# Kernel tuning notes

Hardware: AMD Instinct MI355X
Metric: run time of the kernel (lower is better)

The kernel has to match this reference:

```python
import jax, jax.numpy as jnp
import numpy as np

H = 8      # num_heads
DH = 80    # head_dim = embed_dim // num_heads


def setup_inputs() -> dict:
    key = jax.random.key(0)
    ks = jax.random.split(key, 7)
    B, T, S = 8, 4096, 77
    hidden, embed, ctx = 640, 640, 768
    sc_h = 1.0 / np.sqrt(hidden)
    sc_c = 1.0 / np.sqrt(ctx)
    sc_e = 1.0 / np.sqrt(embed)
    return {
        "tokens": jax.random.normal(ks[0], (B, T, hidden), jnp.float32),
        "context": jax.random.normal(ks[1], (B, S, ctx), jnp.float32),
        "Wq": jax.random.normal(ks[2], (hidden, embed), jnp.float32) * sc_h,
        "Wk": jax.random.normal(ks[3], (ctx, embed), jnp.float32) * sc_c,
        "Wv": jax.random.normal(ks[4], (ctx, embed), jnp.float32) * sc_c,
        "Wo": jax.random.normal(ks[5], (embed, hidden), jnp.float32) * sc_e,
        "bo": jnp.zeros((hidden,), jnp.float32),
    }


def reference(tokens, context, Wq, Wk, Wv, Wo, bo):
    B, T, _ = tokens.shape
    S = context.shape[1]
    Q = (tokens @ Wq).reshape(B, T, H, DH)    # B T H D
    K = (context @ Wk).reshape(B, S, H, DH)   # B S H D
    V = (context @ Wv).reshape(B, S, H, DH)
    scores = jnp.einsum('bthd,bshd->bhts', Q, K) / jnp.sqrt(jnp.float32(DH))
    attn = jax.nn.softmax(scores, axis=-1)    # B H T S
    ctx_vecs = jnp.einsum('bhts,bshd->bthd', attn, V).reshape(B, T, H * DH)
    return ctx_vecs @ Wo + bo
```

## Files before the change

kernel.cpp:

```cpp
#include <hip/hip_runtime.h>
#include <hip/hip_bf16.h>
#include <hip/hip_fp16.h>

typedef __attribute__((ext_vector_type(4))) float f32x4;
typedef __attribute__((ext_vector_type(8))) _Float16 f16x8;
typedef __attribute__((ext_vector_type(8))) unsigned short u16x8;

__device__ __forceinline__ unsigned short f2h(float f) {
    _Float16 h = (_Float16)f;
    return __builtin_bit_cast(unsigned short, h);
}

#define GLOAD_LDS16(gp, lp) __builtin_amdgcn_global_load_lds( \
    (const __attribute__((address_space(1))) void*)(gp), \
    (__attribute__((address_space(3))) void*)(lp), 16, 0, 0)
#define PRIO1() __builtin_amdgcn_s_setprio(1)
#define PRIO0() __builtin_amdgcn_s_setprio(0)

__global__ void cvt_kernel(const float* __restrict__ in, ushort* __restrict__ out, int n4) {
    int stride = gridDim.x * blockDim.x;
    for (int i = blockIdx.x * blockDim.x + threadIdx.x; i < n4; i += stride) {
        float4 v = ((const float4*)in)[i];
        ushort4 o;
        o.x = f2h(v.x); o.y = f2h(v.y); o.z = f2h(v.z); o.w = f2h(v.w);
        ((ushort4*)out)[i] = o;
    }
}

__global__ void transpose_cvt2(const float* __restrict__ Wk, const float* __restrict__ Wv,
                               ushort* __restrict__ WkvT) {
    __shared__ float tile[32][33];
    const int z = blockIdx.z;
    const float* src = z ? Wv : Wk;
    ushort* dst = WkvT + (size_t)z * 640 * 768;
    const int R = 768, C = 640;
    int tx = threadIdx.x, ty = threadIdx.y;
    int c = blockIdx.x * 32 + tx;
    int r0 = blockIdx.y * 32;
#pragma unroll
    for (int i = ty; i < 32; i += 8) {
        int r = r0 + i;
        tile[i][tx] = (r < R && c < C) ? src[(size_t)r * C + c] : 0.f;
    }
    __syncthreads();
    int rr = r0 + tx;
    int c0 = blockIdx.x * 32;
#pragma unroll
    for (int i = ty; i < 32; i += 8) {
        int cc = c0 + i;
        if (cc < C && rr < R) dst[(size_t)cc * R + rr] = f2h(tile[tx][i]);
    }
}

__global__ void pack_wfrag(const float* __restrict__ W, ushort* __restrict__ WF) {
    int g = blockIdx.x * 256 + threadIdx.x;
    if (g >= 51200) return;
    int lane = g & 63;
    int fi = (g >> 6) % 10;
    int kt = ((g >> 6) / 10) % 10;
    int h  = (g >> 6) / 100;
    int ni = fi >> 1, kk = fi & 1;
    int n  = h * 80 + ni * 16 + (lane & 15);
    int k0 = kt * 64 + kk * 32 + (lane >> 4) * 8;
    u16x8 o;
#pragma unroll
    for (int e = 0; e < 8; ++e) o[e] = f2h(W[(size_t)(k0 + e) * 640 + n]);
    *(u16x8*)&WF[(size_t)g * 8] = o;
}

__global__ void pack_kvfrag(const ushort* __restrict__ KVb,
                            ushort* __restrict__ KF, ushort* __restrict__ VF) {
    int g = blockIdx.x * 256 + threadIdx.x;
    if (g >= 61440) return;
    int lane = g & 63;
    int fi = (g >> 6) % 15;
    int bh = (g >> 6) / 15;
    int b = bh >> 3, h = bh & 7;
    int ni = fi / 3, kk = fi % 3;
    int l15 = lane & 15, lhi = lane >> 4;
    int sr = ni * 16 + l15; if (sr > 76) sr = 76;
    int d0 = kk * 32 + lhi * 8;
    u16x8 ko, vo;
#pragma unroll
    for (int e = 0; e < 8; ++e)
        ko[e] = KVb[((size_t)b * 77 + sr) * 1280 + h * 80 + d0 + e];
    int dv = ni * 16 + l15;
    int s0 = kk * 32 + lhi * 8;
#pragma unroll
    for (int e = 0; e < 8; ++e) {
        int s = s0 + e;
        vo[e] = (s < 77) ? KVb[((size_t)b * 77 + s) * 1280 + 640 + h * 80 + dv] : (ushort)0;
    }
    *(u16x8*)&KF[(size_t)g * 8] = ko;
    *(u16x8*)&VF[(size_t)g * 8] = vo;
}

template<int OUT_F16, int HAS_BIAS>
__global__ __launch_bounds__(256) void gemm_bt(
    const ushort* __restrict__ A, const ushort* __restrict__ Bt,
    void* __restrict__ C, const float* __restrict__ bias,
    int M, int N, int K)
{
    __shared__ ushort As[128 * 64];
    __shared__ ushort Bs[128 * 64];
    const int tid = threadIdx.x;
    const int lane = tid & 63;
    const int w = tid >> 6;
    const int wr = (w >> 1) * 64, wc = (w & 1) * 64;
    const int m0 = blockIdx.x * 128, n0 = blockIdx.y * 128;
    const int l15 = lane & 15, lhi = lane >> 4;

    f32x4 acc[4][4] = {};

    for (int k0 = 0; k0 < K; k0 += 64) {
        __syncthreads();
#pragma unroll
        for (int i = 0; i < 4; ++i) {
            int c = i * 256 + tid;
            int m = m0 + (c >> 3);
            if (m > M - 1) m = M - 1;
            GLOAD_LDS16(A + (size_t)m * K + k0 + (c & 7) * 8, &As[c * 8]);
        }
#pragma unroll
        for (int i = 0; i < 4; ++i) {
            int c = i * 256 + tid;
            GLOAD_LDS16(Bt + (size_t)(n0 + (c >> 3)) * K + k0 + (c & 7) * 8, &Bs[c * 8]);
        }
        __syncthreads();
#pragma unroll
        for (int kk = 0; kk < 2; ++kk) {
            f16x8 af[4], bfr[4];
#pragma unroll
            for (int mi = 0; mi < 4; ++mi)
                af[mi] = *(const f16x8*)&As[(wr + mi * 16 + l15) * 64 + kk * 32 + lhi * 8];
#pragma unroll
            for (int ni = 0; ni < 4; ++ni)
                bfr[ni] = *(const f16x8*)&Bs[(wc + ni * 16 + l15) * 64 + kk * 32 + lhi * 8];
#pragma unroll
            for (int mi = 0; mi < 4; ++mi)
#pragma unroll
                for (int ni = 0; ni < 4; ++ni)
                    acc[mi][ni] = __builtin_amdgcn_mfma_f32_16x16x32_f16(
                        af[mi], bfr[ni], acc[mi][ni], 0, 0, 0);
        }
    }

#pragma unroll
    for (int mi = 0; mi < 4; ++mi)
#pragma unroll
        for (int ni = 0; ni < 4; ++ni)
#pragma unroll
            for (int r = 0; r < 4; ++r) {
                int row = m0 + wr + mi * 16 + lhi * 4 + r;
                int col = n0 + wc + ni * 16 + l15;
                if (row < M) {
                    float v = acc[mi][ni][r];
                    if (HAS_BIAS) v += bias[col];
                    if (OUT_F16) ((ushort*)C)[(size_t)row * N + col] = f2h(v);
                    else         ((float*)C)[(size_t)row * N + col] = v;
                }
            }
}

__global__ __launch_bounds__(512, 2) void fused_attn(
    const float* __restrict__ tokens, const ushort* __restrict__ WqF,
    const ushort* __restrict__ KF, const ushort* __restrict__ VF,
    const ushort* __restrict__ WoF, const float* __restrict__ bo,
    float* __restrict__ out)
{
    __shared__ __align__(16) ushort lds[40960];
    const int tid = threadIdx.x;
    const int lane = tid & 63;
    const int w = tid >> 6;
    const int l15 = lane & 15, lhi = lane >> 4;
    const int tt = blockIdx.x, b = blockIdx.y;
    const size_t rowbase = (size_t)b * 4096 + (size_t)tt * 64;

    const ushort* WqFb = WqF + (size_t)w * 10 * 5120;
    const ushort* WoFb = WoF + (size_t)w * 10 * 5120;
    const ushort* KFb  = KF + (size_t)(b * 8 + w) * 15 * 512;
    const ushort* VFb  = VF + (size_t)(b * 8 + w) * 15 * 512;

    const int srow = tid >> 3;
    const int sc8  = tid & 7;
    {
        const float* tbase = tokens + (rowbase + srow) * 640 + sc8 * 8;
        float4 sA[4], sB[4];
#pragma unroll
        for (int kt = 0; kt < 4; ++kt) {
            sA[kt] = ((const float4*)(tbase + kt * 64))[0];
            sB[kt] = ((const float4*)(tbase + kt * 64))[1];
        }
#pragma unroll
        for (int kt = 0; kt < 10; ++kt) {
            const int sl = kt & 3;
            u16x8 o;
            o[0]=f2h(sA[sl].x); o[1]=f2h(sA[sl].y); o[2]=f2h(sA[sl].z); o[3]=f2h(sA[sl].w);
            o[4]=f2h(sB[sl].x); o[5]=f2h(sB[sl].y); o[6]=f2h(sB[sl].z); o[7]=f2h(sB[sl].w);
            *(u16x8*)&lds[srow * 640 + (kt * 8 + (sc8 ^ (srow & 7))) * 8] = o;
            if (kt + 4 < 10) {
                sA[sl] = ((const float4*)(tbase + (kt + 4) * 64))[0];
                sB[sl] = ((const float4*)(tbase + (kt + 4) * 64))[1];
            }
        }
    }
    f16x8 BbE[10], BbO[10];
#pragma unroll
    for (int f = 0; f < 10; ++f)
        BbE[f] = *(const f16x8*)(WqFb + f * 512 + lane * 8);
    __syncthreads();

    f32x4 qacc[4][5] = {};
#define QSTEP(BCUR, BNXT, KT) do { \
    const int kt_ = (KT); \
    if (kt_ < 9) { \
        _Pragma("unroll") for (int f = 0; f < 10; ++f) \
            (BNXT)[f] = *(const f16x8*)(WqFb + (size_t)(kt_+1)*5120 + f*512 + lane*8); \
    } \
    _Pragma("unroll") for (int kk = 0; kk < 2; ++kk) { \
        f16x8 af[4]; \
        _Pragma("unroll") for (int mi = 0; mi < 4; ++mi) { \
            int row_ = mi*16 + l15; \
            af[mi] = *(const f16x8*)&lds[row_*640 + (kt_*8 + ((kk*4 + lhi) ^ (row_ & 7)))*8]; \
        } \
        PRIO1(); \
        _Pragma("unroll") for (int mi = 0; mi < 4; ++mi) \
        _Pragma("unroll") for (int ni = 0; ni < 5; ++ni) \
            qacc[mi][ni] = __builtin_amdgcn_mfma_f32_16x16x32_f16(af[mi], (BCUR)[ni*2+kk], qacc[mi][ni], 0, 0, 0); \
        PRIO0(); \
    } \
} while (0)
    for (int kp = 0; kp < 5; ++kp) {
        QSTEP(BbE, BbO, 2*kp);
        QSTEP(BbO, BbE, 2*kp + 1);
    }
#undef QSTEP
    __syncthreads();

    const int qoff = w * 5120;
#pragma unroll
    for (int mi = 0; mi < 4; ++mi)
#pragma unroll
        for (int ni = 0; ni < 5; ++ni)
#pragma unroll
            for (int r = 0; r < 4; ++r)
                lds[qoff + (mi*16 + lhi*4 + r)*80 + ni*16 + l15] = f2h(qacc[mi][ni][r]);
    __builtin_amdgcn_sched_barrier(0);

    const f16x8 zf = {};
    f32x4 sa[4][5] = {};
    {
        f16x8 bk[15];
#pragma unroll
        for (int f = 0; f < 15; ++f)
            bk[f] = *(const f16x8*)(KFb + f * 512 + lane * 8);
#pragma unroll
        for (int kk = 0; kk < 3; ++kk) {
            f16x8 aq[4];
            const int kcol = (kk < 2) ? (kk*32 + lhi*8) : (64 + (lhi & 1)*8);
#pragma unroll
            for (int mi = 0; mi < 4; ++mi) {
                aq[mi] = *(const f16x8*)&lds[qoff + (mi*16 + l15)*80 + kcol];
                if (kk == 2 && lhi >= 2) aq[mi] = zf;
            }
            PRIO1();
#pragma unroll
            for (int mi = 0; mi < 4; ++mi)
#pragma unroll
                for (int ni = 0; ni < 5; ++ni)
                    sa[mi][ni] = __builtin_amdgcn_mfma_f32_16x16x32_f16(aq[mi], bk[ni*3+kk], sa[mi][ni], 0, 0, 0);
            PRIO0();
        }
    }
    __builtin_amdgcn_sched_barrier(0);

    const float sc = 0.11180339887498949f;
#pragma unroll
    for (int mi = 0; mi < 4; ++mi)
#pragma unroll
        for (int r = 0; r < 4; ++r) {
            float v0 = sa[mi][0][r]*sc, v1 = sa[mi][1][r]*sc, v2 = sa[mi][2][r]*sc,
                  v3 = sa[mi][3][r]*sc, v4 = sa[mi][4][r]*sc;
            bool ok4 = l15 < 13;
            float mx = fmaxf(fmaxf(v0, v1), fmaxf(v2, v3));
            if (ok4) mx = fmaxf(mx, v4);
#pragma unroll
            for (int off = 1; off < 16; off <<= 1) mx = fmaxf(mx, __shfl_xor(mx, off, 16));
            float p0 = __expf(v0-mx), p1 = __expf(v1-mx), p2 = __expf(v2-mx), p3 = __expf(v3-mx);
            float p4 = ok4 ? __expf(v4-mx) : 0.f;
            float sm = p0+p1+p2+p3+p4;
#pragma unroll
            for (int off = 1; off < 16; off <<= 1) sm += __shfl_xor(sm, off, 16);
            float inv = 1.f / sm;
            int row = mi*16 + lhi*4 + r;
            lds[qoff + row*80 + 0*16 + l15] = f2h(p0*inv);
            lds[qoff + row*80 + 1*16 + l15] = f2h(p1*inv);
            lds[qoff + row*80 + 2*16 + l15] = f2h(p2*inv);
            lds[qoff + row*80 + 3*16 + l15] = f2h(p3*inv);
            lds[qoff + row*80 + 4*16 + l15] = f2h(p4*inv);
        }
    __builtin_amdgcn_sched_barrier(0);

    f32x4 oa[4][5] = {};
    {
        f16x8 bv[15];
#pragma unroll
        for (int f = 0; f < 15; ++f)
            bv[f] = *(const f16x8*)(VFb + f * 512 + lane * 8);
#pragma unroll
        for (int kk = 0; kk < 3; ++kk) {
            f16x8 ap[4];
            const int kcol = (kk < 2) ? (kk*32 + lhi*8) : (64 + (lhi & 1)*8);
#pragma unroll
            for (int mi = 0; mi < 4; ++mi) {
                ap[mi] = *(const f16x8*)&lds[qoff + (mi*16 + l15)*80 + kcol];
                if (kk == 2 && lhi >= 2) ap[mi] = zf;
            }
            PRIO1();
#pragma unroll
            for (int mi = 0; mi < 4; ++mi)
#pragma unroll
                for (int ni = 0; ni < 5; ++ni)
                    oa[mi][ni] = __builtin_amdgcn_mfma_f32_16x16x32_f16(ap[mi], bv[ni*3+kk], oa[mi][ni], 0, 0, 0);
            PRIO0();
        }
    }
    __syncthreads();

#pragma unroll
    for (int mi = 0; mi < 4; ++mi)
#pragma unroll
        for (int ni = 0; ni < 5; ++ni)
#pragma unroll
            for (int r = 0; r < 4; ++r) {
                int row = mi*16 + lhi*4 + r;
                int col = w*80 + ni*16 + l15;
                int slot = col >> 3;
                int phys = (((slot & ~7) | ((slot ^ row) & 7)) << 3) | (col & 7);
                lds[row*640 + phys] = f2h(oa[mi][ni][r]);
            }
    __syncthreads();

    f32x4 cacc[4][5] = {};
#pragma unroll
    for (int f = 0; f < 10; ++f)
        BbE[f] = *(const f16x8*)(WoFb + f * 512 + lane * 8);
#define OSTEP(BCUR, BNXT, KT) do { \
    const int kt_ = (KT); \
    if (kt_ < 9) { \
        _Pragma("unroll") for (int f = 0; f < 10; ++f) \
            (BNXT)[f] = *(const f16x8*)(WoFb + (size_t)(kt_+1)*5120 + f*512 + lane*8); \
    } \
    _Pragma("unroll") for (int kk = 0; kk < 2; ++kk) { \
        f16x8 af[4]; \
        _Pragma("unroll") for (int mi = 0; mi < 4; ++mi) { \
            int row_ = mi*16 + l15; \
            af[mi] = *(const f16x8*)&lds[row_*640 + (kt_*8 + ((kk*4 + lhi) ^ (row_ & 7)))*8]; \
        } \
        PRIO1(); \
        _Pragma("unroll") for (int mi = 0; mi < 4; ++mi) \
        _Pragma("unroll") for (int ni = 0; ni < 5; ++ni) \
            cacc[mi][ni] = __builtin_amdgcn_mfma_f32_16x16x32_f16(af[mi], (BCUR)[ni*2+kk], cacc[mi][ni], 0, 0, 0); \
        PRIO0(); \
    } \
} while (0)
    for (int kp = 0; kp < 5; ++kp) {
        OSTEP(BbE, BbO, 2*kp);
        OSTEP(BbO, BbE, 2*kp + 1);
    }
#undef OSTEP

#pragma unroll
    for (int ni = 0; ni < 5; ++ni) {
        int col = w*80 + ni*16 + l15;
        float bvl = bo[col];
#pragma unroll
        for (int mi = 0; mi < 4; ++mi)
#pragma unroll
            for (int r = 0; r < 4; ++r)
                out[(rowbase + mi*16 + lhi*4 + r) * 640 + col] = cacc[mi][ni][r] + bvl;
    }
}

extern "C" void kernel_launch(void* const* d_in, const int* in_sizes, int n_in,
                              void* d_out, int out_size, void* d_ws, size_t ws_size,
                              hipStream_t stream) {
    (void)in_sizes; (void)n_in; (void)out_size; (void)ws_size;
    const float* tokens  = (const float*)d_in[0];
    const float* context = (const float*)d_in[1];
    const float* Wq = (const float*)d_in[2];
    const float* Wk = (const float*)d_in[3];
    const float* Wv = (const float*)d_in[4];
    const float* Wo = (const float*)d_in[5];
    const float* bo = (const float*)d_in[6];
    float* out = (float*)d_out;

    ushort* ws   = (ushort*)d_ws;
    ushort* ctx16 = ws;
    ushort* WkvT = ctx16 + (size_t)616 * 768;
    ushort* KVb  = WkvT + (size_t)1280 * 768;
    ushort* WqF  = KVb  + (size_t)616 * 1280;
    ushort* WoF  = WqF  + (size_t)640 * 640;
    ushort* KF   = WoF  + (size_t)640 * 640;
    ushort* VF   = KF   + (size_t)61440 * 8;

    cvt_kernel<<<462, 256, 0, stream>>>(context, ctx16, 616 * 768 / 4);
    transpose_cvt2<<<dim3(20, 24, 2), dim3(32, 8), 0, stream>>>(Wk, Wv, WkvT);
    pack_wfrag<<<200, 256, 0, stream>>>(Wq, WqF);
    pack_wfrag<<<200, 256, 0, stream>>>(Wo, WoF);
    gemm_bt<1, 0><<<dim3(5, 10), 256, 0, stream>>>(ctx16, WkvT, KVb, nullptr, 616, 1280, 768);
    pack_kvfrag<<<240, 256, 0, stream>>>(KVb, KF, VF);
    fused_attn<<<dim3(64, 8), 512, 0, stream>>>(tokens, WqF, KF, VF, WoF, bo, out);
}
```

Measured before the change: 123.6 us.

## Halve fused attention row tile to 32 rows and double grid

Each block of the fused attention kernel now handles 32 token rows instead of 64. This halves LDS use and accumulator registers, and the grid doubles to 1024 blocks. Weight fragment prefetch now goes at half-k granularity (5 fragments per step instead of 10), which lowers register pressure further. The aim is higher occupancy and better latency hiding. In exchange, every block reloads the full Wq/Wo weights and K/V fragments, which doubles total weight traffic, and each MFMA batch is smaller.

Result: slower. 129.8 us (+5.0%).

```diff
diff --git a/kernel.cpp b/kernel.cpp
--- a/kernel.cpp
+++ b/kernel.cpp
@@ -168,78 +168,72 @@
     const ushort* __restrict__ WoF, const float* __restrict__ bo,
     float* __restrict__ out)
 {
-    __shared__ __align__(16) ushort lds[40960];
+    __shared__ __align__(16) ushort lds[20480];
     const int tid = threadIdx.x;
     const int lane = tid & 63;
     const int w = tid >> 6;
     const int l15 = lane & 15, lhi = lane >> 4;
     const int tt = blockIdx.x, b = blockIdx.y;
-    const size_t rowbase = (size_t)b * 4096 + (size_t)tt * 64;
+    const size_t rowbase = (size_t)b * 4096 + (size_t)tt * 32;
 
     const ushort* WqFb = WqF + (size_t)w * 10 * 5120;
     const ushort* WoFb = WoF + (size_t)w * 10 * 5120;
     const ushort* KFb  = KF + (size_t)(b * 8 + w) * 15 * 512;
     const ushort* VFb  = VF + (size_t)(b * 8 + w) * 15 * 512;
 
-    const int srow = tid >> 3;
-    const int sc8  = tid & 7;
     {
-        const float* tbase = tokens + (rowbase + srow) * 640 + sc8 * 8;
-        float4 sA[4], sB[4];
-#pragma unroll
-        for (int kt = 0; kt < 4; ++kt) {
-            sA[kt] = ((const float4*)(tbase + kt * 64))[0];
-            sB[kt] = ((const float4*)(tbase + kt * 64))[1];
-        }
-#pragma unroll
-        for (int kt = 0; kt < 10; ++kt) {
-            const int sl = kt & 3;
+        const int srow = tid >> 4;
+        const int c16  = tid & 15;
+        const float* tbase = tokens + (rowbase + srow) * 640 + c16 * 8;
+        float4 sA[5], sB[5];
+#pragma unroll
+        for (int i = 0; i < 5; ++i) {
+            sA[i] = ((const float4*)(tbase + i * 128))[0];
+            sB[i] = ((const float4*)(tbase + i * 128))[1];
+        }
+#pragma unroll
+        for (int i = 0; i < 5; ++i) {
+            int slot = i * 16 + c16;
+            int phys = (slot & ~7) | ((slot ^ srow) & 7);
             u16x8 o;
-            o[0]=f2h(sA[sl].x); o[1]=f2h(sA[sl].y); o[2]=f2h(sA[sl].z); o[3]=f2h(sA[sl].w);
-            o[4]=f2h(sB[sl].x); o[5]=f2h(sB[sl].y); o[6]=f2h(sB[sl].z); o[7]=f2h(sB[sl].w);
-            *(u16x8*)&lds[srow * 640 + (kt * 8 + (sc8 ^ (srow & 7))) * 8] = o;
-            if (kt + 4 < 10) {
-                sA[sl] = ((const float4*)(tbase + (kt + 4) * 64))[0];
-                sB[sl] = ((const float4*)(tbase + (kt + 4) * 64))[1];
-            }
-        }
-    }
-    f16x8 BbE[10], BbO[10];
-#pragma unroll
-    for (int f = 0; f < 10; ++f)
-        BbE[f] = *(const f16x8*)(WqFb + f * 512 + lane * 8);
-    __syncthreads();
-
-    f32x4 qacc[4][5] = {};
-#define QSTEP(BCUR, BNXT, KT) do { \
-    const int kt_ = (KT); \
-    if (kt_ < 9) { \
-        _Pragma("unroll") for (int f = 0; f < 10; ++f) \
-            (BNXT)[f] = *(const f16x8*)(WqFb + (size_t)(kt_+1)*5120 + f*512 + lane*8); \
+            o[0]=f2h(sA[i].x); o[1]=f2h(sA[i].y); o[2]=f2h(sA[i].z); o[3]=f2h(sA[i].w);
+            o[4]=f2h(sB[i].x); o[5]=f2h(sB[i].y); o[6]=f2h(sB[i].z); o[7]=f2h(sB[i].w);
+            *(u16x8*)&lds[srow * 640 + phys * 8] = o;
+        }
+    }
+    f16x8 PE[5], PO[5];
+#pragma unroll
+    for (int f = 0; f < 5; ++f)
+        PE[f] = *(const f16x8*)(WqFb + (f * 2) * 512 + lane * 8);
+    __syncthreads();
+
+    f32x4 qacc[2][5] = {};
+#define GHALF(ACC, PC, PN, WB, KT, KK, NKT, NKK, DOPF) do { \
+    if (DOPF) { \
+        _Pragma("unroll") for (int f = 0; f < 5; ++f) \
+            (PN)[f] = *(const f16x8*)((WB) + (size_t)(NKT) * 5120 + (f * 2 + (NKK)) * 512 + lane * 8); \
     } \
-    _Pragma("unroll") for (int kk = 0; kk < 2; ++kk) { \
-        f16x8 af[4]; \
-        _Pragma("unroll") for (int mi = 0; mi < 4; ++mi) { \
-            int row_ = mi*16 + l15; \
-            af[mi] = *(const f16x8*)&lds[row_*640 + (kt_*8 + ((kk*4 + lhi) ^ (row_ & 7)))*8]; \
-        } \
-        PRIO1(); \
-        _Pragma("unroll") for (int mi = 0; mi < 4; ++mi) \
-        _Pragma("unroll") for (int ni = 0; ni < 5; ++ni) \
-            qacc[mi][ni] = __builtin_amdgcn_mfma_f32_16x16x32_f16(af[mi], (BCUR)[ni*2+kk], qacc[mi][ni], 0, 0, 0); \
-        PRIO0(); \
+    f16x8 af[2]; \
+    _Pragma("unroll") for (int mi = 0; mi < 2; ++mi) { \
+        int row_ = mi * 16 + l15; \
+        af[mi] = *(const f16x8*)&lds[row_ * 640 + ((KT) * 8 + (((KK) * 4 + lhi) ^ (row_ & 7))) * 8]; \
     } \
+    PRIO1(); \
+    _Pragma("unroll") for (int mi = 0; mi < 2; ++mi) \
+    _Pragma("unroll") for (int ni = 0; ni < 5; ++ni) \
+        (ACC)[mi][ni] = __builtin_amdgcn_mfma_f32_16x16x32_f16(af[mi], (PC)[ni], (ACC)[mi][ni], 0, 0, 0); \
+    PRIO0(); \
 } while (0)
-    for (int kp = 0; kp < 5; ++kp) {
-        QSTEP(BbE, BbO, 2*kp);
-        QSTEP(BbO, BbE, 2*kp + 1);
-    }
-#undef QSTEP
-    __syncthreads();
-
-    const int qoff = w * 5120;
-#pragma unroll
-    for (int mi = 0; mi < 4; ++mi)
+
+    for (int kt = 0; kt < 10; ++kt) {
+        GHALF(qacc, PE, PO, WqFb, kt, 0, kt, 1, 1);
+        GHALF(qacc, PO, PE, WqFb, kt, 1, kt + 1, 0, kt < 9);
+    }
+    __syncthreads();
+
+    const int qoff = w * 2560;
+#pragma unroll
+    for (int mi = 0; mi < 2; ++mi)
 #pragma unroll
         for (int ni = 0; ni < 5; ++ni)
 #pragma unroll
@@ -248,35 +242,36 @@
     __builtin_amdgcn_sched_barrier(0);
 
     const f16x8 zf = {};
-    f32x4 sa[4][5] = {};
-    {
-        f16x8 bk[15];
-#pragma unroll
-        for (int f = 0; f < 15; ++f)
-            bk[f] = *(const f16x8*)(KFb + f * 512 + lane * 8);
-#pragma unroll
-        for (int kk = 0; kk < 3; ++kk) {
-            f16x8 aq[4];
-            const int kcol = (kk < 2) ? (kk*32 + lhi*8) : (64 + (lhi & 1)*8);
-#pragma unroll
-            for (int mi = 0; mi < 4; ++mi) {
-                aq[mi] = *(const f16x8*)&lds[qoff + (mi*16 + l15)*80 + kcol];
-                if (kk == 2 && lhi >= 2) aq[mi] = zf;
-            }
-            PRIO1();
-#pragma unroll
-            for (int mi = 0; mi < 4; ++mi)
-#pragma unroll
-                for (int ni = 0; ni < 5; ++ni)
-                    sa[mi][ni] = __builtin_amdgcn_mfma_f32_16x16x32_f16(aq[mi], bk[ni*3+kk], sa[mi][ni], 0, 0, 0);
-            PRIO0();
-        }
-    }
+    f32x4 sa[2][5] = {};
+#define ATT_KK(ACC, PC, PN, FB, KK, NKK, DOPF) do { \
+    if (DOPF) { \
+        _Pragma("unroll") for (int f = 0; f < 5; ++f) \
+            (PN)[f] = *(const f16x8*)((FB) + (f * 3 + (NKK)) * 512 + lane * 8); \
+    } \
+    f16x8 aq[2]; \
+    const int kcol = ((KK) < 2) ? ((KK)*32 + lhi*8) : (64 + (lhi & 1)*8); \
+    _Pragma("unroll") for (int mi = 0; mi < 2; ++mi) { \
+        aq[mi] = *(const f16x8*)&lds[qoff + (mi*16 + l15)*80 + kcol]; \
+        if ((KK) == 2 && lhi >= 2) aq[mi] = zf; \
+    } \
+    PRIO1(); \
+    _Pragma("unroll") for (int mi = 0; mi < 2; ++mi) \
+    _Pragma("unroll") for (int ni = 0; ni < 5; ++ni) \
+        (ACC)[mi][ni] = __builtin_amdgcn_mfma_f32_16x16x32_f16(aq[mi], (PC)[ni], (ACC)[mi][ni], 0, 0, 0); \
+    PRIO0(); \
+} while (0)
+
+#pragma unroll
+    for (int f = 0; f < 5; ++f)
+        PE[f] = *(const f16x8*)(KFb + (f * 3) * 512 + lane * 8);
+    ATT_KK(sa, PE, PO, KFb, 0, 1, 1);
+    ATT_KK(sa, PO, PE, KFb, 1, 2, 1);
+    ATT_KK(sa, PE, PO, KFb, 2, 0, 0);
     __builtin_amdgcn_sched_barrier(0);
 
     const float sc = 0.11180339887498949f;
 #pragma unroll
-    for (int mi = 0; mi < 4; ++mi)
+    for (int mi = 0; mi < 2; ++mi)
 #pragma unroll
         for (int r = 0; r < 4; ++r) {
             float v0 = sa[mi][0][r]*sc, v1 = sa[mi][1][r]*sc, v2 = sa[mi][2][r]*sc,
@@ -301,34 +296,18 @@
         }
     __builtin_amdgcn_sched_barrier(0);
 
-    f32x4 oa[4][5] = {};
-    {
-        f16x8 bv[15];
-#pragma unroll
-        for (int f = 0; f < 15; ++f)
-            bv[f] = *(const f16x8*)(VFb + f * 512 + lane * 8);
-#pragma unroll
-        for (int kk = 0; kk < 3; ++kk) {
-            f16x8 ap[4];
-            const int kcol = (kk < 2) ? (kk*32 + lhi*8) : (64 + (lhi & 1)*8);
-#pragma unroll
-            for (int mi = 0; mi < 4; ++mi) {
-                ap[mi] = *(const f16x8*)&lds[qoff + (mi*16 + l15)*80 + kcol];
-                if (kk == 2 && lhi >= 2) ap[mi] = zf;
-            }
-            PRIO1();
-#pragma unroll
-            for (int mi = 0; mi < 4; ++mi)
-#pragma unroll
-                for (int ni = 0; ni < 5; ++ni)
-                    oa[mi][ni] = __builtin_amdgcn_mfma_f32_16x16x32_f16(ap[mi], bv[ni*3+kk], oa[mi][ni], 0, 0, 0);
-            PRIO0();
-        }
-    }
-    __syncthreads();
-
-#pragma unroll
-    for (int mi = 0; mi < 4; ++mi)
+    f32x4 oa[2][5] = {};
+#pragma unroll
+    for (int f = 0; f < 5; ++f)
+        PE[f] = *(const f16x8*)(VFb + (f * 3) * 512 + lane * 8);
+    ATT_KK(oa, PE, PO, VFb, 0, 1, 1);
+    ATT_KK(oa, PO, PE, VFb, 1, 2, 1);
+    ATT_KK(oa, PE, PO, VFb, 2, 0, 0);
+#undef ATT_KK
+    __syncthreads();
+
+#pragma unroll
+    for (int mi = 0; mi < 2; ++mi)
 #pragma unroll
         for (int ni = 0; ni < 5; ++ni)
 #pragma unroll
@@ -336,46 +315,27 @@
                 int row = mi*16 + lhi*4 + r;
                 int col = w*80 + ni*16 + l15;
                 int slot = col >> 3;
-                int phys = (((slot & ~7) | ((slot ^ row) & 7)) << 3) | (col & 7);
-                lds[row*640 + phys] = f2h(oa[mi][ni][r]);
+                int phys = (slot & ~7) | ((slot ^ row) & 7);
+                lds[row*640 + phys*8 + (col & 7)] = f2h(oa[mi][ni][r]);
             }
     __syncthreads();
 
-    f32x4 cacc[4][5] = {};
-#pragma unroll
-    for (int f = 0; f < 10; ++f)
-        BbE[f] = *(const f16x8*)(WoFb + f * 512 + lane * 8);
-#define OSTEP(BCUR, BNXT, KT) do { \
-    const int kt_ = (KT); \
-    if (kt_ < 9) { \
-        _Pragma("unroll") for (int f = 0; f < 10; ++f) \
-            (BNXT)[f] = *(const f16x8*)(WoFb + (size_t)(kt_+1)*5120 + f*512 + lane*8); \
-    } \
-    _Pragma("unroll") for (int kk = 0; kk < 2; ++kk) { \
-        f16x8 af[4]; \
-        _Pragma("unroll") for (int mi = 0; mi < 4; ++mi) { \
-            int row_ = mi*16 + l15; \
-            af[mi] = *(const f16x8*)&lds[row_*640 + (kt_*8 + ((kk*4 + lhi) ^ (row_ & 7)))*8]; \
-        } \
-        PRIO1(); \
-        _Pragma("unroll") for (int mi = 0; mi < 4; ++mi) \
-        _Pragma("unroll") for (int ni = 0; ni < 5; ++ni) \
-            cacc[mi][ni] = __builtin_amdgcn_mfma_f32_16x16x32_f16(af[mi], (BCUR)[ni*2+kk], cacc[mi][ni], 0, 0, 0); \
-        PRIO0(); \
-    } \
-} while (0)
-    for (int kp = 0; kp < 5; ++kp) {
-        OSTEP(BbE, BbO, 2*kp);
-        OSTEP(BbO, BbE, 2*kp + 1);
-    }
-#undef OSTEP
+    f32x4 cacc[2][5] = {};
+#pragma unroll
+    for (int f = 0; f < 5; ++f)
+        PE[f] = *(const f16x8*)(WoFb + (f * 2) * 512 + lane * 8);
+    for (int kt = 0; kt < 10; ++kt) {
+        GHALF(cacc, PE, PO, WoFb, kt, 0, kt, 1, 1);
+        GHALF(cacc, PO, PE, WoFb, kt, 1, kt + 1, 0, kt < 9);
+    }
+#undef GHALF
 
 #pragma unroll
     for (int ni = 0; ni < 5; ++ni) {
         int col = w*80 + ni*16 + l15;
         float bvl = bo[col];
 #pragma unroll
-        for (int mi = 0; mi < 4; ++mi)
+        for (int mi = 0; mi < 2; ++mi)
 #pragma unroll
             for (int r = 0; r < 4; ++r)
                 out[(rowbase + mi*16 + lhi*4 + r) * 640 + col] = cacc[mi][ni][r] + bvl;
@@ -410,5 +370,5 @@
     pack_wfrag<<<200, 256, 0, stream>>>(Wo, WoF);
     gemm_bt<1, 0><<<dim3(5, 10), 256, 0, stream>>>(ctx16, WkvT, KVb, nullptr, 616, 1280, 768);
     pack_kvfrag<<<240, 256, 0, stream>>>(KVb, KF, VF);
-    fused_attn<<<dim3(64, 8), 512, 0, stream>>>(tokens, WqF, KF, VF, WoF, bo, out);
-}
+    fused_attn<<<dim3(128, 8), 512, 0, stream>>>(tokens, WqF, KF, VF, WoF, bo, out);
+}
```
